# Optimization experiments

Hardware: AMD Instinct MI355X
Metric: run time of the kernel (lower is better)

The kernel has to match this reference:

```python
import jax, jax.numpy as jnp
import numpy as np

N, D, H, E_DIM = 2048, 128, 8, 10
DH = D // H
EPS = 1e-5

def _ln(x, g, b):
    mu = jnp.mean(x, axis=-1, keepdims=True)
    var = jnp.mean((x - mu) ** 2, axis=-1, keepdims=True)
    return (x - mu) / jnp.sqrt(var + EPS) * g + b

def setup_inputs() -> dict:
    key = jax.random.key(0)
    ks = jax.random.split(key, 16)
    E = 65536
    inp = {
        "node_feat": jax.random.normal(ks[0], (N, D), jnp.float32),
        "edge_feat": jax.random.normal(ks[1], (E, E_DIM), jnp.float32),
        "src": jax.random.randint(ks[2], (E,), 0, N, jnp.int32).astype(jnp.int64),
        "dst": jax.random.randint(ks[3], (E,), 0, N, jnp.int32).astype(jnp.int64),
        "Wq": jax.random.normal(ks[4], (D, D), jnp.float32) * 0.02,
        "bq": jnp.zeros((D,), jnp.float32),
        "Wk": jax.random.normal(ks[5], (D, D), jnp.float32) * 0.02,
        "bk": jnp.zeros((D,), jnp.float32),
        "Wv": jax.random.normal(ks[6], (D, D), jnp.float32) * 0.02,
        "bv": jnp.zeros((D,), jnp.float32),
        "Wo": jax.random.normal(ks[7], (D, D), jnp.float32) * 0.02,
        "bo": jnp.zeros((D,), jnp.float32),
        "We": jax.random.normal(ks[8], (E_DIM, H), jnp.float32) * 0.02,
        "be": jnp.zeros((H,), jnp.float32),
        "g1": jnp.ones((D,), jnp.float32),
        "b1n": jnp.zeros((D,), jnp.float32),
        "g2": jnp.ones((D,), jnp.float32),
        "b2n": jnp.zeros((D,), jnp.float32),
        "W1": jax.random.normal(ks[9], (D, 4 * D), jnp.float32) * 0.02,
        "bf1": jnp.zeros((4 * D,), jnp.float32),
        "W2": jax.random.normal(ks[10], (4 * D, D), jnp.float32) * 0.02,
        "bf2": jnp.zeros((D,), jnp.float32),
    }
    return inp

def reference(node_feat, edge_feat, src, dst, Wq, bq, Wk, bk, Wv, bv, Wo, bo,
              We, be, g1, b1n, g2, b2n, W1, bf1, W2, bf2):
    n = node_feat.shape[0]
    Q = (node_feat @ Wq + bq).reshape(n, H, DH)
    K = (node_feat @ Wk + bk).reshape(n, H, DH)
    V = (node_feat @ Wv + bv).reshape(n, H, DH)
    scores = jnp.einsum('ihd,jhd->ijh', Q, K) / jnp.sqrt(jnp.float32(DH))
    # scatter edge bias into dense [N,N,H] (set semantics, like torch indexed assign)
    edge_bias = edge_feat @ We + be  # [E,H]
    bias = jnp.zeros((n, n, H), scores.dtype).at[src, dst].set(edge_bias)
    scores = scores + bias
    # symmetric adjacency mask with self-loops
    adj = jnp.zeros((n, n), scores.dtype)
    adj = adj.at[src, dst].set(1.0).at[dst, src].set(1.0)
    idx = jnp.arange(n)
    adj = adj.at[idx, idx].set(1.0)
    scores = jnp.where(adj[:, :, None] == 0, -jnp.inf, scores)
    attn = jax.nn.softmax(scores, axis=1)  # softmax over keys j (dim=1)
    out = jnp.einsum('ijh,jhd->ihd', attn, V).reshape(n, -1)
    out = out @ Wo + bo
    out = _ln(out + node_feat, g1, b1n)
    ffn = jax.nn.relu(out @ W1 + bf1) @ W2 + bf2
    out = _ln(out + ffn, g2, b2n)
    return out
```

## Files before the change

### kernel.cpp

```cpp
#include <hip/hip_runtime.h>
#include <hip/hip_bf16.h>

#define NN   2048
#define DDIM 128
#define HH   8
#define DHH  16
#define NEDGE 65536
#define FFN  512
#define EPSV 1e-5f
#define CAP  256

typedef const float* fp_c;

__device__ __forceinline__ bool idx64(const int* src) {
    return (src[1] | src[3] | src[5] | src[7] | src[9] | src[11]) == 0;
}

__global__ __launch_bounds__(512) void k_pq(float* Qf, float* Kf, float* Vf, fp_c x,
                                            fp_c Wq, fp_c bq, fp_c Wk, fp_c bk, fp_c Wv, fp_c bv,
                                            int* ewin, unsigned* bm, float* eb,
                                            const int* src, const int* dst,
                                            fp_c edge_feat, fp_c We, fp_c be) {
    int b = blockIdx.x;
    int t = threadIdx.x;
    if (b < 256) {
        __shared__ float sx[8][DDIM];
        __shared__ float redq[4][8][DDIM];
        __shared__ float redk[4][8][DDIM];
        __shared__ float redv[4][8][DDIM];
        int r0 = b * 8;
        int c = t & 127;
        int ks = t >> 7;
        sx[t >> 7][t & 127]       = x[r0 * DDIM + t];
        sx[4 + (t >> 7)][t & 127] = x[r0 * DDIM + 512 + t];
        __syncthreads();
        float aq[8], ak[8], av[8];
#pragma unroll
        for (int r = 0; r < 8; r++) { aq[r] = 0; ak[r] = 0; av[r] = 0; }
        int kbeg = ks * 32;
#pragma unroll 8
        for (int k = kbeg; k < kbeg + 32; k++) {
            float wq = Wq[k * DDIM + c];
            float wk = Wk[k * DDIM + c];
            float wv = Wv[k * DDIM + c];
#pragma unroll
            for (int r = 0; r < 8; r++) {
                float xv = sx[r][k];
                aq[r] += xv * wq; ak[r] += xv * wk; av[r] += xv * wv;
            }
        }
#pragma unroll
        for (int r = 0; r < 8; r++) {
            redq[ks][r][c] = aq[r];
            redk[ks][r][c] = ak[r];
            redv[ks][r][c] = av[r];
        }
        __syncthreads();
        int rr = t >> 7, cc = t & 127;
        float vq0 = 0, vk0 = 0, vv0 = 0, vq1 = 0, vk1 = 0, vv1 = 0;
#pragma unroll
        for (int s = 0; s < 4; s++) {
            vq0 += redq[s][rr][cc];     vk0 += redk[s][rr][cc];     vv0 += redv[s][rr][cc];
            vq1 += redq[s][rr + 4][cc]; vk1 += redk[s][rr + 4][cc]; vv1 += redv[s][rr + 4][cc];
        }
        float vbq = bq[cc], vbk = bk[cc], vbv = bv[cc];
        Qf[(r0 + rr) * DDIM + cc]     = (vq0 + vbq) * 0.25f;
        Kf[(r0 + rr) * DDIM + cc]     = vk0 + vbk;
        Vf[(r0 + rr) * DDIM + cc]     = vv0 + vbv;
        Qf[(r0 + rr + 4) * DDIM + cc] = (vq1 + vbq) * 0.25f;
        Kf[(r0 + rr + 4) * DDIM + cc] = vk1 + vbk;
        Vf[(r0 + rr + 4) * DDIM + cc] = vv1 + vbv;
    } else {
        __shared__ float sWe[80];
        __shared__ float sbe[8];
        if (t < 80) sWe[t] = We[t];
        if (t < 8)  sbe[t] = be[t];
        __syncthreads();
        int u = (b - 256) * 512 + t;
        if (u < NN * 64 / 4) ((int4*)bm)[u] = make_int4(0, 0, 0, 0);
        ((int4*)ewin)[u]         = make_int4(0, 0, 0, 0);
        ((int4*)ewin)[u + 65536] = make_int4(0, 0, 0, 0);
        if (u < NEDGE) {
            float ef[10];
#pragma unroll
            for (int k = 0; k < 10; k++) ef[k] = edge_feat[u * 10 + k];
#pragma unroll
            for (int h = 0; h < 8; h++) {
                float a = sbe[h];
#pragma unroll
                for (int k = 0; k < 10; k++) a += ef[k] * sWe[k * 8 + h];
                eb[u * 8 + h] = a;
            }
        }
    }
}

__global__ __launch_bounds__(512) void k_scatter(unsigned* bm, const int* src, const int* dst) {
    int t = blockIdx.x * blockDim.x + threadIdx.x;
    bool is64 = idx64(src);
    if (t < NEDGE) {
        int s = is64 ? src[2 * t] : src[t];
        int d = is64 ? dst[2 * t] : dst[t];
        atomicOr(&bm[s * 64 + (d >> 5)], 1u << (d & 31));
        atomicOr(&bm[d * 64 + (s >> 5)], 1u << (s & 31));
    } else if (t < NEDGE + NN) {
        int i = t - NEDGE;
        atomicOr(&bm[i * 64 + (i >> 5)], 1u << (i & 31));
    }
}

__global__ __launch_bounds__(512) void k_rank(int* ewin, const unsigned* bm,
                                              const int* src, const int* dst) {
    int e = blockIdx.x * blockDim.x + threadIdx.x;
    if (e >= NEDGE) return;
    bool is64 = idx64(src);
    int s = is64 ? src[2 * e] : src[e];
    int d = is64 ? dst[2 * e] : dst[e];
    const unsigned* row = bm + s * 64;
    int dw = d >> 5;
    int rank = __popc(row[dw] & ((1u << (d & 31)) - 1u));
    for (int w = 0; w < dw; w++) rank += __popc(row[w]);
    atomicMax(&ewin[s * CAP + rank], e + 1);
}

__global__ __launch_bounds__(256) void k_attn(float* attn_out, const float* Qf, const float* Kf,
                                              const float* Vf, const int* ewin, const float* eb,
                                              const unsigned* bm) {
    __shared__ float qrow[DDIM];
    __shared__ int   lj[CAP + 8];
    __shared__ int   lev[CAP + 8];
    __shared__ float sc[CAP + 8][HH];
    __shared__ float hinv[HH];
    __shared__ float redpv[2][DDIM];
    __shared__ int   scnt;
    int i = blockIdx.x;
    int t = threadIdx.x;
    if (t < 128) qrow[t] = Qf[i * DDIM + t];

    if (t < 64) {
        unsigned word = bm[i * 64 + t];
        int pc = __popc(word);
        int x = pc;
#pragma unroll
        for (int off = 1; off < 64; off <<= 1) {
            int y = __shfl_up(x, off);
            if (t >= off) x += y;
        }
        int cnt = __shfl(x, 63);
        if (cnt > CAP - 8) cnt = CAP - 8;
        int idx = x - pc;
        unsigned w = word;
        while (w && idx < CAP) {
            int bpos = __ffs(w) - 1;
            lj[idx++] = (t << 5) + bpos;
            w &= w - 1;
        }
        if (t < 8) lj[cnt + t] = 0;
        if (t == 0) scnt = cnt;
    }
    __syncthreads();
    int cnt = scnt;
    int cnt8 = (cnt + 7) & ~7;
    if (t < cnt8) lev[t] = (t < cnt) ? (ewin[i * CAP + t] - 1) : -1;
    __syncthreads();

    int h = t & 7;
    int nsl = t >> 3;
    const float4* q4 = (const float4*)(qrow + h * DHH);
    float4 q0 = q4[0], q1 = q4[1], q2 = q4[2], q3 = q4[3];
    for (int n = nsl; n < cnt8; n += 32) {
        int j = lj[n];
        const float4* k4 = (const float4*)(Kf + j * DDIM + h * DHH);
        float4 k0 = k4[0], k1 = k4[1], k2 = k4[2], k3 = k4[3];
        float s = q0.x * k0.x + q0.y * k0.y + q0.z * k0.z + q0.w * k0.w
                + q1.x * k1.x + q1.y * k1.y + q1.z * k1.z + q1.w * k1.w
                + q2.x * k2.x + q2.y * k2.y + q2.z * k2.z + q2.w * k2.w
                + q3.x * k3.x + q3.y * k3.y + q3.z * k3.z + q3.w * k3.w;
        int ev = lev[n];
        if (ev >= 0) s += eb[ev * 8 + h];
        sc[n][h] = s;
    }
    __syncthreads();

    {
        int hh = t >> 5;
        int sub = t & 31;
        float m = -1e30f;
        for (int n = sub; n < cnt; n += 32) m = fmaxf(m, sc[n][hh]);
#pragma unroll
        for (int off = 1; off < 32; off <<= 1) m = fmaxf(m, __shfl_xor(m, off));
        float ssum = 0.f;
        for (int n = sub; n < cnt; n += 32) {
            float e = __expf(sc[n][hh] - m);
            sc[n][hh] = e;
            ssum += e;
        }
#pragma unroll
        for (int off = 1; off < 32; off <<= 1) ssum += __shfl_xor(ssum, off);
        if (sub == 0) hinv[hh] = 1.0f / ssum;
    }
    if (t < 64) {
        int p = cnt + (t >> 3);
        if (p < cnt8) sc[p][t & 7] = 0.f;
    }
    __syncthreads();

    {
        int g = t >> 7, c = t & 127, h2 = c >> 4;
        float a = 0.f;
#pragma unroll 4
        for (int n = g; n < cnt8; n += 2)
            a += sc[n][h2] * Vf[lj[n] * DDIM + c];
        redpv[g][c] = a;
    }
    __syncthreads();
    if (t < 128)
        attn_out[i * DDIM + t] = (redpv[0][t] + redpv[1][t]) * hinv[t >> 4];
}

__global__ __launch_bounds__(512) void k_tail(float* out, const float* ain,
                                              fp_c Wo, fp_c bo, fp_c node, fp_c g1, fp_c b1,
                                              fp_c W1, fp_c bf1, fp_c W2, fp_c bf2,
                                              fp_c g2, fp_c b2) {
    __shared__ float sa[8][DDIM];
    __shared__ float red[4][8][DDIM];
    __shared__ float x1ld[8][DDIM];
    __shared__ float sh[8][FFN];
    __shared__ float4 sc4[8];
    int t = threadIdx.x;
    int r0 = blockIdx.x * 8;
    int c = t & 127;
    int ks = t >> 7;
    int rr = t >> 7, cc = t & 127;
    sa[t >> 7][t & 127]       = ain[r0 * DDIM + t];
    sa[4 + (t >> 7)][t & 127] = ain[r0 * DDIM + 512 + t];
    __syncthreads();

    {
        float acc[8] = {0, 0, 0, 0, 0, 0, 0, 0};
        int kbeg = ks * 32;
#pragma unroll 8
        for (int k = kbeg; k < kbeg + 32; k++) {
            float w = Wo[k * DDIM + c];
#pragma unroll
            for (int r = 0; r < 8; r++) acc[r] += sa[r][k] * w;
        }
#pragma unroll
        for (int r = 0; r < 8; r++) red[ks][r][c] = acc[r];
        __syncthreads();
        float bov = bo[cc];
        float val0 = red[0][rr][cc] + red[1][rr][cc] + red[2][rr][cc] + red[3][rr][cc]
                   + bov + node[(r0 + rr) * DDIM + cc];
        float val1 = red[0][rr + 4][cc] + red[1][rr + 4][cc] + red[2][rr + 4][cc] + red[3][rr + 4][cc]
                   + bov + node[(r0 + rr + 4) * DDIM + cc];
        float4 v = make_float4(val0, val0 * val0, val1, val1 * val1);
#pragma unroll
        for (int off = 32; off >= 1; off >>= 1) {
            v.x += __shfl_down(v.x, off);
            v.y += __shfl_down(v.y, off);
            v.z += __shfl_down(v.z, off);
            v.w += __shfl_down(v.w, off);
        }
        if ((t & 63) == 0) sc4[t >> 6] = v;
        __syncthreads();
        float gv = g1[cc], bv = b1[cc];
        {
            float sum = sc4[2 * rr].x + sc4[2 * rr + 1].x;
            float sq  = sc4[2 * rr].y + sc4[2 * rr + 1].y;
            float mu = sum * (1.0f / DDIM);
            float var = sq * (1.0f / DDIM) - mu * mu;
            x1ld[rr][cc] = (val0 - mu) * rsqrtf(var + EPSV) * gv + bv;
        }
        {
            float sum = sc4[2 * rr].z + sc4[2 * rr + 1].z;
            float sq  = sc4[2 * rr].w + sc4[2 * rr + 1].w;
            float mu = sum * (1.0f / DDIM);
            float var = sq * (1.0f / DDIM) - mu * mu;
            x1ld[rr + 4][cc] = (val1 - mu) * rsqrtf(var + EPSV) * gv + bv;
        }
    }
    __syncthreads();

    {
        float acc[8] = {0, 0, 0, 0, 0, 0, 0, 0};
#pragma unroll 4
        for (int k = 0; k < DDIM; k++) {
            float w = W1[k * FFN + t];
#pragma unroll
            for (int r = 0; r < 8; r++) acc[r] += x1ld[r][k] * w;
        }
        float bb = bf1[t];
#pragma unroll
        for (int r = 0; r < 8; r++) sh[r][t] = fmaxf(acc[r] + bb, 0.f);
    }
    __syncthreads();

    {
        float acc[8] = {0, 0, 0, 0, 0, 0, 0, 0};
        int kbeg = ks * 128;
#pragma unroll 8
        for (int k = kbeg; k < kbeg + 128; k++) {
            float w = W2[k * DDIM + c];
#pragma unroll
            for (int r = 0; r < 8; r++) acc[r] += sh[r][k] * w;
        }
#pragma unroll
        for (int r = 0; r < 8; r++) red[ks][r][c] = acc[r];
        __syncthreads();
        float bv2 = bf2[cc];
        float val0 = red[0][rr][cc] + red[1][rr][cc] + red[2][rr][cc] + red[3][rr][cc]
                   + bv2 + x1ld[rr][cc];
        float val1 = red[0][rr + 4][cc] + red[1][rr + 4][cc] + red[2][rr + 4][cc] + red[3][rr + 4][cc]
                   + bv2 + x1ld[rr + 4][cc];
        float4 v = make_float4(val0, val0 * val0, val1, val1 * val1);
#pragma unroll
        for (int off = 32; off >= 1; off >>= 1) {
            v.x += __shfl_down(v.x, off);
            v.y += __shfl_down(v.y, off);
            v.z += __shfl_down(v.z, off);
            v.w += __shfl_down(v.w, off);
        }
        if ((t & 63) == 0) sc4[t >> 6] = v;
        __syncthreads();
        float gv = g2[cc], bv = b2[cc];
        {
            float sum = sc4[2 * rr].x + sc4[2 * rr + 1].x;
            float sq  = sc4[2 * rr].y + sc4[2 * rr + 1].y;
            float mu = sum * (1.0f / DDIM);
            float var = sq * (1.0f / DDIM) - mu * mu;
            out[(r0 + rr) * DDIM + cc] = (val0 - mu) * rsqrtf(var + EPSV) * gv + bv;
        }
        {
            float sum = sc4[2 * rr].z + sc4[2 * rr + 1].z;
            float sq  = sc4[2 * rr].w + sc4[2 * rr + 1].w;
            float mu = sum * (1.0f / DDIM);
            float var = sq * (1.0f / DDIM) - mu * mu;
            out[(r0 + rr + 4) * DDIM + cc] = (val1 - mu) * rsqrtf(var + EPSV) * gv + bv;
        }
    }
}

extern "C" void kernel_launch(void* const* d_in, const int* in_sizes, int n_in,
                              void* d_out, int out_size, void* d_ws, size_t ws_size,
                              hipStream_t stream) {
    fp_c node = (fp_c)d_in[0];
    fp_c edge_feat = (fp_c)d_in[1];
    const int* src = (const int*)d_in[2];
    const int* dst = (const int*)d_in[3];
    fp_c Wq = (fp_c)d_in[4];  fp_c bq = (fp_c)d_in[5];
    fp_c Wk = (fp_c)d_in[6];  fp_c bk = (fp_c)d_in[7];
    fp_c Wv = (fp_c)d_in[8];  fp_c bv = (fp_c)d_in[9];
    fp_c Wo = (fp_c)d_in[10]; fp_c bo = (fp_c)d_in[11];
    fp_c We = (fp_c)d_in[12]; fp_c be = (fp_c)d_in[13];
    fp_c g1 = (fp_c)d_in[14]; fp_c b1n = (fp_c)d_in[15];
    fp_c g2 = (fp_c)d_in[16]; fp_c b2n = (fp_c)d_in[17];
    fp_c W1 = (fp_c)d_in[18]; fp_c bf1 = (fp_c)d_in[19];
    fp_c W2 = (fp_c)d_in[20]; fp_c bf2 = (fp_c)d_in[21];

    char* ws = (char*)d_ws;
    int* ewin     = (int*)ws;      ws += (size_t)NN * CAP * 4;
    unsigned* bm  = (unsigned*)ws; ws += (size_t)NN * 64 * 4;
    float* eb     = (float*)ws;    ws += (size_t)NEDGE * 8 * 4;
    float* Qf     = (float*)ws;    ws += (size_t)NN * DDIM * 4;
    float* Kf     = (float*)ws;    ws += (size_t)NN * DDIM * 4;
    float* Vf     = (float*)ws;    ws += (size_t)NN * DDIM * 4;
    float* attn_o = (float*)ws;    ws += (size_t)NN * DDIM * 4;

    k_pq<<<384, 512, 0, stream>>>(Qf, Kf, Vf, node, Wq, bq, Wk, bk, Wv, bv,
                                  ewin, bm, eb, src, dst, edge_feat, We, be);
    k_scatter<<<(NEDGE + NN + 511) / 512, 512, 0, stream>>>(bm, src, dst);
    k_rank<<<NEDGE / 512, 512, 0, stream>>>(ewin, bm, src, dst);
    k_attn<<<NN, 256, 0, stream>>>(attn_o, Qf, Kf, Vf, ewin, eb, bm);
    k_tail<<<NN / 8, 512, 0, stream>>>((float*)d_out, attn_o, Wo, bo, node, g1, b1n,
                                       W1, bf1, W2, bf2, g2, b2n);
}
```

Before: 81.33 us.

## Fuse all stages into one cooperative persistent kernel with dense edge-id table

```diff
diff --git a/kernel.cpp b/kernel.cpp
--- a/kernel.cpp
+++ b/kernel.cpp
@@ -1,258 +1,231 @@
 #include <hip/hip_runtime.h>
 #include <hip/hip_bf16.h>
-
-#define NN   2048
-#define DDIM 128
-#define HH   8
-#define DHH  16
+#include <hip/hip_cooperative_groups.h>
+
+namespace cg = cooperative_groups;
+
+#define NN    2048
+#define DDIM  128
+#define HH    8
+#define DHH   16
 #define NEDGE 65536
-#define FFN  512
-#define EPSV 1e-5f
-#define CAP  256
-
-typedef const float* fp_c;
+#define FFN   512
+#define EPSV  1e-5f
+#define CAP   256
+#define NBLK  256
+#define NTHR  512
+
+struct Params {
+    const float *node, *edge_feat;
+    const int *src, *dst;
+    const float *Wq, *bq, *Wk, *bk, *Wv, *bv, *Wo, *bo, *We, *be;
+    const float *g1, *b1n, *g2n, *b2n, *W1, *bf1, *W2, *bf2;
+    float *Qf, *Kf, *Vf, *out;
+    int* eid;
+    unsigned* bm;
+    float* eb;
+};
+
+union Smem {
+    struct { float sx[8][DDIM]; float rq[4][8][DDIM]; float rk[4][8][DDIM];
+             float rv[4][8][DDIM]; } q;
+    struct { float qrow[2][DDIM]; int lj[2][CAP + 8]; int lev[2][CAP + 8];
+             float sc[2][CAP + 8][HH]; float hinv[2][HH];
+             float redpv[2][2][DDIM]; int scnt[2]; } a;
+    struct { float red[4][8][DDIM]; float x1[8][DDIM]; float sh[8][FFN];
+             float4 sc4[8]; } tl;
+};
+struct Pers { float ao[8][DDIM]; };
 
 __device__ __forceinline__ bool idx64(const int* src) {
     return (src[1] | src[3] | src[5] | src[7] | src[9] | src[11]) == 0;
 }
 
-__global__ __launch_bounds__(512) void k_pq(float* Qf, float* Kf, float* Vf, fp_c x,
-                                            fp_c Wq, fp_c bq, fp_c Wk, fp_c bk, fp_c Wv, fp_c bv,
-                                            int* ewin, unsigned* bm, float* eb,
-                                            const int* src, const int* dst,
-                                            fp_c edge_feat, fp_c We, fp_c be) {
-    int b = blockIdx.x;
-    int t = threadIdx.x;
-    if (b < 256) {
-        __shared__ float sx[8][DDIM];
-        __shared__ float redq[4][8][DDIM];
-        __shared__ float redk[4][8][DDIM];
-        __shared__ float redv[4][8][DDIM];
-        int r0 = b * 8;
-        int c = t & 127;
-        int ks = t >> 7;
-        sx[t >> 7][t & 127]       = x[r0 * DDIM + t];
-        sx[4 + (t >> 7)][t & 127] = x[r0 * DDIM + 512 + t];
-        __syncthreads();
-        float aq[8], ak[8], av[8];
-#pragma unroll
-        for (int r = 0; r < 8; r++) { aq[r] = 0; ak[r] = 0; av[r] = 0; }
-        int kbeg = ks * 32;
+__device__ __forceinline__ void phase_pq(const Params& P, int b, int t, Smem& S, bool is64) {
+    int g = b * NTHR + t;
+    if (g < NN * 64 / 4) ((int4*)P.bm)[g] = make_int4(0, 0, 0, 0);
+    if (g < NN) P.eid[(long)g * NN + g] = -2;
+    if (g < NEDGE) {
+        int s = is64 ? P.src[2 * g] : P.src[g];
+        int d = is64 ? P.dst[2 * g] : P.dst[g];
+        P.eid[(long)s * NN + d] = -2;
+        P.eid[(long)d * NN + s] = -2;
+        float ef[10];
+#pragma unroll
+        for (int k = 0; k < 10; k++) ef[k] = P.edge_feat[g * 10 + k];
+#pragma unroll
+        for (int h = 0; h < 8; h++) {
+            float a = P.be[h];
+#pragma unroll
+            for (int k = 0; k < 10; k++) a += ef[k] * P.We[k * 8 + h];
+            P.eb[g * 8 + h] = a;
+        }
+    }
+    int r0 = b * 8, c = t & 127, ks = t >> 7;
+    S.q.sx[ks][c]     = P.node[r0 * DDIM + t];
+    S.q.sx[4 + ks][c] = P.node[r0 * DDIM + 512 + t];
+    __syncthreads();
+    float aq[8], ak[8], av[8];
+#pragma unroll
+    for (int r = 0; r < 8; r++) { aq[r] = 0; ak[r] = 0; av[r] = 0; }
+    int kbeg = ks * 32;
 #pragma unroll 8
-        for (int k = kbeg; k < kbeg + 32; k++) {
-            float wq = Wq[k * DDIM + c];
-            float wk = Wk[k * DDIM + c];
-            float wv = Wv[k * DDIM + c];
-#pragma unroll
-            for (int r = 0; r < 8; r++) {
-                float xv = sx[r][k];
-                aq[r] += xv * wq; ak[r] += xv * wk; av[r] += xv * wv;
+    for (int k = kbeg; k < kbeg + 32; k++) {
+        float wq = P.Wq[k * DDIM + c];
+        float wk = P.Wk[k * DDIM + c];
+        float wv = P.Wv[k * DDIM + c];
+#pragma unroll
+        for (int r = 0; r < 8; r++) {
+            float xv = S.q.sx[r][k];
+            aq[r] += xv * wq; ak[r] += xv * wk; av[r] += xv * wv;
+        }
+    }
+#pragma unroll
+    for (int r = 0; r < 8; r++) {
+        S.q.rq[ks][r][c] = aq[r];
+        S.q.rk[ks][r][c] = ak[r];
+        S.q.rv[ks][r][c] = av[r];
+    }
+    __syncthreads();
+    int rr = t >> 7, cc = t & 127;
+    float vq0 = 0, vk0 = 0, vv0 = 0, vq1 = 0, vk1 = 0, vv1 = 0;
+#pragma unroll
+    for (int s = 0; s < 4; s++) {
+        vq0 += S.q.rq[s][rr][cc];     vk0 += S.q.rk[s][rr][cc];     vv0 += S.q.rv[s][rr][cc];
+        vq1 += S.q.rq[s][rr + 4][cc]; vk1 += S.q.rk[s][rr + 4][cc]; vv1 += S.q.rv[s][rr + 4][cc];
+    }
+    float vbq = P.bq[cc], vbk = P.bk[cc], vbv = P.bv[cc];
+    P.Qf[(r0 + rr) * DDIM + cc]     = (vq0 + vbq) * 0.25f;
+    P.Kf[(r0 + rr) * DDIM + cc]     = vk0 + vbk;
+    P.Vf[(r0 + rr) * DDIM + cc]     = vv0 + vbv;
+    P.Qf[(r0 + rr + 4) * DDIM + cc] = (vq1 + vbq) * 0.25f;
+    P.Kf[(r0 + rr + 4) * DDIM + cc] = vk1 + vbk;
+    P.Vf[(r0 + rr + 4) * DDIM + cc] = vv1 + vbv;
+}
+
+__device__ __forceinline__ void phase_scatter(const Params& P, int b, int t, bool is64) {
+    int g = b * NTHR + t;
+    if (g < NEDGE) {
+        int s = is64 ? P.src[2 * g] : P.src[g];
+        int d = is64 ? P.dst[2 * g] : P.dst[g];
+        atomicOr(&P.bm[s * 64 + (d >> 5)], 1u << (d & 31));
+        atomicOr(&P.bm[d * 64 + (s >> 5)], 1u << (s & 31));
+        atomicMax(&P.eid[(long)s * NN + d], g);
+    } else if (g < NEDGE + NN) {
+        int i = g - NEDGE;
+        atomicOr(&P.bm[i * 64 + (i >> 5)], 1u << (i & 31));
+    }
+}
+
+__device__ __forceinline__ void phase_attn(const Params& P, int b, int t, Smem& S, Pers& Pr) {
+    int gi = t >> 8;
+    int t2 = t & 255;
+#pragma unroll 1
+    for (int p = 0; p < 4; p++) {
+        __syncthreads();
+        int il = p * 2 + gi;
+        int i = b * 8 + il;
+        if (t2 < 128) S.a.qrow[gi][t2] = P.Qf[i * DDIM + t2];
+        if (t2 < 64) {
+            unsigned word = P.bm[i * 64 + t2];
+            int pc = __popc(word);
+            int x = pc;
+#pragma unroll
+            for (int off = 1; off < 64; off <<= 1) {
+                int y = __shfl_up(x, off);
+                if (t2 >= off) x += y;
             }
-        }
-#pragma unroll
-        for (int r = 0; r < 8; r++) {
-            redq[ks][r][c] = aq[r];
-            redk[ks][r][c] = ak[r];
-            redv[ks][r][c] = av[r];
-        }
-        __syncthreads();
-        int rr = t >> 7, cc = t & 127;
-        float vq0 = 0, vk0 = 0, vv0 = 0, vq1 = 0, vk1 = 0, vv1 = 0;
-#pragma unroll
-        for (int s = 0; s < 4; s++) {
-            vq0 += redq[s][rr][cc];     vk0 += redk[s][rr][cc];     vv0 += redv[s][rr][cc];
-            vq1 += redq[s][rr + 4][cc]; vk1 += redk[s][rr + 4][cc]; vv1 += redv[s][rr + 4][cc];
-        }
-        float vbq = bq[cc], vbk = bk[cc], vbv = bv[cc];
-        Qf[(r0 + rr) * DDIM + cc]     = (vq0 + vbq) * 0.25f;
-        Kf[(r0 + rr) * DDIM + cc]     = vk0 + vbk;
-        Vf[(r0 + rr) * DDIM + cc]     = vv0 + vbv;
-        Qf[(r0 + rr + 4) * DDIM + cc] = (vq1 + vbq) * 0.25f;
-        Kf[(r0 + rr + 4) * DDIM + cc] = vk1 + vbk;
-        Vf[(r0 + rr + 4) * DDIM + cc] = vv1 + vbv;
-    } else {
-        __shared__ float sWe[80];
-        __shared__ float sbe[8];
-        if (t < 80) sWe[t] = We[t];
-        if (t < 8)  sbe[t] = be[t];
-        __syncthreads();
-        int u = (b - 256) * 512 + t;
-        if (u < NN * 64 / 4) ((int4*)bm)[u] = make_int4(0, 0, 0, 0);
-        ((int4*)ewin)[u]         = make_int4(0, 0, 0, 0);
-        ((int4*)ewin)[u + 65536] = make_int4(0, 0, 0, 0);
-        if (u < NEDGE) {
-            float ef[10];
-#pragma unroll
-            for (int k = 0; k < 10; k++) ef[k] = edge_feat[u * 10 + k];
-#pragma unroll
-            for (int h = 0; h < 8; h++) {
-                float a = sbe[h];
-#pragma unroll
-                for (int k = 0; k < 10; k++) a += ef[k] * sWe[k * 8 + h];
-                eb[u * 8 + h] = a;
+            int cnt = __shfl(x, 63);
+            if (cnt > CAP - 8) cnt = CAP - 8;
+            int idx = x - pc;
+            unsigned w = word;
+            while (w && idx < CAP) {
+                int bp = __ffs(w) - 1;
+                S.a.lj[gi][idx++] = (t2 << 5) + bp;
+                w &= w - 1;
             }
-        }
-    }
-}
-
-__global__ __launch_bounds__(512) void k_scatter(unsigned* bm, const int* src, const int* dst) {
-    int t = blockIdx.x * blockDim.x + threadIdx.x;
-    bool is64 = idx64(src);
-    if (t < NEDGE) {
-        int s = is64 ? src[2 * t] : src[t];
-        int d = is64 ? dst[2 * t] : dst[t];
-        atomicOr(&bm[s * 64 + (d >> 5)], 1u << (d & 31));
-        atomicOr(&bm[d * 64 + (s >> 5)], 1u << (s & 31));
-    } else if (t < NEDGE + NN) {
-        int i = t - NEDGE;
-        atomicOr(&bm[i * 64 + (i >> 5)], 1u << (i & 31));
-    }
-}
-
-__global__ __launch_bounds__(512) void k_rank(int* ewin, const unsigned* bm,
-                                              const int* src, const int* dst) {
-    int e = blockIdx.x * blockDim.x + threadIdx.x;
-    if (e >= NEDGE) return;
-    bool is64 = idx64(src);
-    int s = is64 ? src[2 * e] : src[e];
-    int d = is64 ? dst[2 * e] : dst[e];
-    const unsigned* row = bm + s * 64;
-    int dw = d >> 5;
-    int rank = __popc(row[dw] & ((1u << (d & 31)) - 1u));
-    for (int w = 0; w < dw; w++) rank += __popc(row[w]);
-    atomicMax(&ewin[s * CAP + rank], e + 1);
-}
-
-__global__ __launch_bounds__(256) void k_attn(float* attn_out, const float* Qf, const float* Kf,
-                                              const float* Vf, const int* ewin, const float* eb,
-                                              const unsigned* bm) {
-    __shared__ float qrow[DDIM];
-    __shared__ int   lj[CAP + 8];
-    __shared__ int   lev[CAP + 8];
-    __shared__ float sc[CAP + 8][HH];
-    __shared__ float hinv[HH];
-    __shared__ float redpv[2][DDIM];
-    __shared__ int   scnt;
-    int i = blockIdx.x;
-    int t = threadIdx.x;
-    if (t < 128) qrow[t] = Qf[i * DDIM + t];
-
-    if (t < 64) {
-        unsigned word = bm[i * 64 + t];
-        int pc = __popc(word);
-        int x = pc;
-#pragma unroll
-        for (int off = 1; off < 64; off <<= 1) {
-            int y = __shfl_up(x, off);
-            if (t >= off) x += y;
-        }
-        int cnt = __shfl(x, 63);
-        if (cnt > CAP - 8) cnt = CAP - 8;
-        int idx = x - pc;
-        unsigned w = word;
-        while (w && idx < CAP) {
-            int bpos = __ffs(w) - 1;
-            lj[idx++] = (t << 5) + bpos;
-            w &= w - 1;
-        }
-        if (t < 8) lj[cnt + t] = 0;
-        if (t == 0) scnt = cnt;
-    }
-    __syncthreads();
-    int cnt = scnt;
-    int cnt8 = (cnt + 7) & ~7;
-    if (t < cnt8) lev[t] = (t < cnt) ? (ewin[i * CAP + t] - 1) : -1;
-    __syncthreads();
-
-    int h = t & 7;
-    int nsl = t >> 3;
-    const float4* q4 = (const float4*)(qrow + h * DHH);
-    float4 q0 = q4[0], q1 = q4[1], q2 = q4[2], q3 = q4[3];
-    for (int n = nsl; n < cnt8; n += 32) {
-        int j = lj[n];
-        const float4* k4 = (const float4*)(Kf + j * DDIM + h * DHH);
-        float4 k0 = k4[0], k1 = k4[1], k2 = k4[2], k3 = k4[3];
-        float s = q0.x * k0.x + q0.y * k0.y + q0.z * k0.z + q0.w * k0.w
-                + q1.x * k1.x + q1.y * k1.y + q1.z * k1.z + q1.w * k1.w
-                + q2.x * k2.x + q2.y * k2.y + q2.z * k2.z + q2.w * k2.w
-                + q3.x * k3.x + q3.y * k3.y + q3.z * k3.z + q3.w * k3.w;
-        int ev = lev[n];
-        if (ev >= 0) s += eb[ev * 8 + h];
-        sc[n][h] = s;
-    }
-    __syncthreads();
-
-    {
-        int hh = t >> 5;
-        int sub = t & 31;
-        float m = -1e30f;
-        for (int n = sub; n < cnt; n += 32) m = fmaxf(m, sc[n][hh]);
-#pragma unroll
-        for (int off = 1; off < 32; off <<= 1) m = fmaxf(m, __shfl_xor(m, off));
-        float ssum = 0.f;
-        for (int n = sub; n < cnt; n += 32) {
-            float e = __expf(sc[n][hh] - m);
-            sc[n][hh] = e;
-            ssum += e;
-        }
-#pragma unroll
-        for (int off = 1; off < 32; off <<= 1) ssum += __shfl_xor(ssum, off);
-        if (sub == 0) hinv[hh] = 1.0f / ssum;
-    }
-    if (t < 64) {
-        int p = cnt + (t >> 3);
-        if (p < cnt8) sc[p][t & 7] = 0.f;
-    }
-    __syncthreads();
-
-    {
-        int g = t >> 7, c = t & 127, h2 = c >> 4;
-        float a = 0.f;
+            if (t2 < 8) S.a.lj[gi][cnt + t2] = 0;
+            if (t2 == 0) S.a.scnt[gi] = cnt;
+        }
+        __syncthreads();
+        int cnt = S.a.scnt[gi];
+        int cnt8 = (cnt + 7) & ~7;
+        if (t2 < cnt8)
+            S.a.lev[gi][t2] = (t2 < cnt) ? P.eid[(long)i * NN + S.a.lj[gi][t2]] : -1;
+        __syncthreads();
+        {
+            int h = t2 & 7, nsl = t2 >> 3;
+            const float4* q4 = (const float4*)(&S.a.qrow[gi][h * DHH]);
+            float4 q0 = q4[0], q1 = q4[1], q2 = q4[2], q3 = q4[3];
+            for (int n = nsl; n < cnt8; n += 32) {
+                int j = S.a.lj[gi][n];
+                const float4* k4 = (const float4*)(P.Kf + j * DDIM + h * DHH);
+                float4 k0 = k4[0], k1 = k4[1], k2 = k4[2], k3 = k4[3];
+                float s = q0.x * k0.x + q0.y * k0.y + q0.z * k0.z + q0.w * k0.w
+                        + q1.x * k1.x + q1.y * k1.y + q1.z * k1.z + q1.w * k1.w
+                        + q2.x * k2.x + q2.y * k2.y + q2.z * k2.z + q2.w * k2.w
+                        + q3.x * k3.x + q3.y * k3.y + q3.z * k3.z + q3.w * k3.w;
+                int ev = S.a.lev[gi][n];
+                if (ev >= 0) s += P.eb[ev * 8 + h];
+                S.a.sc[gi][n][h] = s;
+            }
+        }
+        __syncthreads();
+        {
+            int hh = t2 >> 5, sub = t2 & 31;
+            float m = -1e30f;
+            for (int n = sub; n < cnt; n += 32) m = fmaxf(m, S.a.sc[gi][n][hh]);
+#pragma unroll
+            for (int off = 1; off < 32; off <<= 1) m = fmaxf(m, __shfl_xor(m, off));
+            float ssum = 0.f;
+            for (int n = sub; n < cnt; n += 32) {
+                float e = __expf(S.a.sc[gi][n][hh] - m);
+                S.a.sc[gi][n][hh] = e;
+                ssum += e;
+            }
+#pragma unroll
+            for (int off = 1; off < 32; off <<= 1) ssum += __shfl_xor(ssum, off);
+            if (sub == 0) S.a.hinv[gi][hh] = 1.0f / ssum;
+        }
+        if (t2 < 64) {
+            int pp = cnt + (t2 >> 3);
+            if (pp < cnt8) S.a.sc[gi][pp][t2 & 7] = 0.f;
+        }
+        __syncthreads();
+        {
+            int gg = t2 >> 7, c = t2 & 127, h2 = c >> 4;
+            float a = 0.f;
 #pragma unroll 4
-        for (int n = g; n < cnt8; n += 2)
-            a += sc[n][h2] * Vf[lj[n] * DDIM + c];
-        redpv[g][c] = a;
-    }
-    __syncthreads();
-    if (t < 128)
-        attn_out[i * DDIM + t] = (redpv[0][t] + redpv[1][t]) * hinv[t >> 4];
-}
-
-__global__ __launch_bounds__(512) void k_tail(float* out, const float* ain,
-                                              fp_c Wo, fp_c bo, fp_c node, fp_c g1, fp_c b1,
-                                              fp_c W1, fp_c bf1, fp_c W2, fp_c bf2,
-                                              fp_c g2, fp_c b2) {
-    __shared__ float sa[8][DDIM];
-    __shared__ float red[4][8][DDIM];
-    __shared__ float x1ld[8][DDIM];
-    __shared__ float sh[8][FFN];
-    __shared__ float4 sc4[8];
-    int t = threadIdx.x;
-    int r0 = blockIdx.x * 8;
-    int c = t & 127;
-    int ks = t >> 7;
+            for (int n = gg; n < cnt8; n += 2)
+                a += S.a.sc[gi][n][h2] * P.Vf[S.a.lj[gi][n] * DDIM + c];
+            S.a.redpv[gi][gg][c] = a;
+        }
+        __syncthreads();
+        if (t2 < 128)
+            Pr.ao[il][t2] = (S.a.redpv[gi][0][t2] + S.a.redpv[gi][1][t2]) * S.a.hinv[gi][t2 >> 4];
+    }
+}
+
+__device__ __forceinline__ void phase_tail(const Params& P, int b, int t, Smem& S, Pers& Pr) {
+    int r0 = b * 8, c = t & 127, ks = t >> 7;
     int rr = t >> 7, cc = t & 127;
-    sa[t >> 7][t & 127]       = ain[r0 * DDIM + t];
-    sa[4 + (t >> 7)][t & 127] = ain[r0 * DDIM + 512 + t];
-    __syncthreads();
-
     {
         float acc[8] = {0, 0, 0, 0, 0, 0, 0, 0};
         int kbeg = ks * 32;
 #pragma unroll 8
         for (int k = kbeg; k < kbeg + 32; k++) {
-            float w = Wo[k * DDIM + c];
-#pragma unroll
-            for (int r = 0; r < 8; r++) acc[r] += sa[r][k] * w;
-        }
-#pragma unroll
-        for (int r = 0; r < 8; r++) red[ks][r][c] = acc[r];
-        __syncthreads();
-        float bov = bo[cc];
-        float val0 = red[0][rr][cc] + red[1][rr][cc] + red[2][rr][cc] + red[3][rr][cc]
-                   + bov + node[(r0 + rr) * DDIM + cc];
-        float val1 = red[0][rr + 4][cc] + red[1][rr + 4][cc] + red[2][rr + 4][cc] + red[3][rr + 4][cc]
-                   + bov + node[(r0 + rr + 4) * DDIM + cc];
+            float w = P.Wo[k * DDIM + c];
+#pragma unroll
+            for (int r = 0; r < 8; r++) acc[r] += Pr.ao[r][k] * w;
+        }
+#pragma unroll
+        for (int r = 0; r < 8; r++) S.tl.red[ks][r][c] = acc[r];
+        __syncthreads();
+        float bov = P.bo[cc];
+        float val0 = S.tl.red[0][rr][cc] + S.tl.red[1][rr][cc] + S.tl.red[2][rr][cc]
+                   + S.tl.red[3][rr][cc] + bov + P.node[(r0 + rr) * DDIM + cc];
+        float val1 = S.tl.red[0][rr + 4][cc] + S.tl.red[1][rr + 4][cc] + S.tl.red[2][rr + 4][cc]
+                   + S.tl.red[3][rr + 4][cc] + bov + P.node[(r0 + rr + 4) * DDIM + cc];
         float4 v = make_float4(val0, val0 * val0, val1, val1 * val1);
 #pragma unroll
         for (int off = 32; off >= 1; off >>= 1) {
@@ -261,57 +234,56 @@
             v.z += __shfl_down(v.z, off);
             v.w += __shfl_down(v.w, off);
         }
-        if ((t & 63) == 0) sc4[t >> 6] = v;
-        __syncthreads();
-        float gv = g1[cc], bv = b1[cc];
-        {
-            float sum = sc4[2 * rr].x + sc4[2 * rr + 1].x;
-            float sq  = sc4[2 * rr].y + sc4[2 * rr + 1].y;
+        if ((t & 63) == 0) S.tl.sc4[t >> 6] = v;
+        __syncthreads();
+        float gv = P.g1[cc], bv = P.b1n[cc];
+        {
+            float sum = S.tl.sc4[2 * rr].x + S.tl.sc4[2 * rr + 1].x;
+            float sq  = S.tl.sc4[2 * rr].y + S.tl.sc4[2 * rr + 1].y;
             float mu = sum * (1.0f / DDIM);
             float var = sq * (1.0f / DDIM) - mu * mu;
-            x1ld[rr][cc] = (val0 - mu) * rsqrtf(var + EPSV) * gv + bv;
-        }
-        {
-            float sum = sc4[2 * rr].z + sc4[2 * rr + 1].z;
-            float sq  = sc4[2 * rr].w + sc4[2 * rr + 1].w;
+            S.tl.x1[rr][cc] = (val0 - mu) * rsqrtf(var + EPSV) * gv + bv;
+        }
+        {
+            float sum = S.tl.sc4[2 * rr].z + S.tl.sc4[2 * rr + 1].z;
+            float sq  = S.tl.sc4[2 * rr].w + S.tl.sc4[2 * rr + 1].w;
             float mu = sum * (1.0f / DDIM);
             float var = sq * (1.0f / DDIM) - mu * mu;
-            x1ld[rr + 4][cc] = (val1 - mu) * rsqrtf(var + EPSV) * gv + bv;
-        }
-    }
-    __syncthreads();
-
+            S.tl.x1[rr + 4][cc] = (val1 - mu) * rsqrtf(var + EPSV) * gv + bv;
+        }
+    }
+    __syncthreads();
     {
         float acc[8] = {0, 0, 0, 0, 0, 0, 0, 0};
 #pragma unroll 4
         for (int k = 0; k < DDIM; k++) {
-            float w = W1[k * FFN + t];
-#pragma unroll
-            for (int r = 0; r < 8; r++) acc[r] += x1ld[r][k] * w;
-        }
-        float bb = bf1[t];
-#pragma unroll
-        for (int r = 0; r < 8; r++) sh[r][t] = fmaxf(acc[r] + bb, 0.f);
-    }
-    __syncthreads();
-
+            float w = P.W1[k * FFN + t];
+#pragma unroll
+            for (int r = 0; r < 8; r++) acc[r] += S.tl.x1[r][k] * w;
+        }
+        float bb = P.bf1[t];
+#pragma unroll
+        for (int r = 0; r < 8; r++) S.tl.sh[r][t] = fmaxf(acc[r] + bb, 0.f);
+    }
+    __syncthreads();
     {
         float acc[8] = {0, 0, 0, 0, 0, 0, 0, 0};
         int kbeg = ks * 128;
 #pragma unroll 8
         for (int k = kbeg; k < kbeg + 128; k++) {
-            float w = W2[k * DDIM + c];
-#pragma unroll
-            for (int r = 0; r < 8; r++) acc[r] += sh[r][k] * w;
-        }
-#pragma unroll
-        for (int r = 0; r < 8; r++) red[ks][r][c] = acc[r];
-        __syncthreads();
-        float bv2 = bf2[cc];
-        float val0 = red[0][rr][cc] + red[1][rr][cc] + red[2][rr][cc] + red[3][rr][cc]
-                   + bv2 + x1ld[rr][cc];
-        float val1 = red[0][rr + 4][cc] + red[1][rr + 4][cc] + red[2][rr + 4][cc] + red[3][rr + 4][cc]
-                   + bv2 + x1ld[rr + 4][cc];
+            float w = P.W2[k * DDIM + c];
+#pragma unroll
+            for (int r = 0; r < 8; r++) acc[r] += S.tl.sh[r][k] * w;
+        }
+        __syncthreads();
+#pragma unroll
+        for (int r = 0; r < 8; r++) S.tl.red[ks][r][c] = acc[r];
+        __syncthreads();
+        float bv2 = P.bf2[cc];
+        float val0 = S.tl.red[0][rr][cc] + S.tl.red[1][rr][cc] + S.tl.red[2][rr][cc]
+                   + S.tl.red[3][rr][cc] + bv2 + S.tl.x1[rr][cc];
+        float val1 = S.tl.red[0][rr + 4][cc] + S.tl.red[1][rr + 4][cc] + S.tl.red[2][rr + 4][cc]
+                   + S.tl.red[3][rr + 4][cc] + bv2 + S.tl.x1[rr + 4][cc];
         float4 v = make_float4(val0, val0 * val0, val1, val1 * val1);
 #pragma unroll
         for (int off = 32; off >= 1; off >>= 1) {
@@ -320,57 +292,97 @@
             v.z += __shfl_down(v.z, off);
             v.w += __shfl_down(v.w, off);
         }
-        if ((t & 63) == 0) sc4[t >> 6] = v;
-        __syncthreads();
-        float gv = g2[cc], bv = b2[cc];
-        {
-            float sum = sc4[2 * rr].x + sc4[2 * rr + 1].x;
-            float sq  = sc4[2 * rr].y + sc4[2 * rr + 1].y;
+        if ((t & 63) == 0) S.tl.sc4[t >> 6] = v;
+        __syncthreads();
+        float gv = P.g2n[cc], bv = P.b2n[cc];
+        {
+            float sum = S.tl.sc4[2 * rr].x + S.tl.sc4[2 * rr + 1].x;
+            float sq  = S.tl.sc4[2 * rr].y + S.tl.sc4[2 * rr + 1].y;
             float mu = sum * (1.0f / DDIM);
             float var = sq * (1.0f / DDIM) - mu * mu;
-            out[(r0 + rr) * DDIM + cc] = (val0 - mu) * rsqrtf(var + EPSV) * gv + bv;
-        }
-        {
-            float sum = sc4[2 * rr].z + sc4[2 * rr + 1].z;
-            float sq  = sc4[2 * rr].w + sc4[2 * rr + 1].w;
+            P.out[(r0 + rr) * DDIM + cc] = (val0 - mu) * rsqrtf(var + EPSV) * gv + bv;
+        }
+        {
+            float sum = S.tl.sc4[2 * rr].z + S.tl.sc4[2 * rr + 1].z;
+            float sq  = S.tl.sc4[2 * rr].w + S.tl.sc4[2 * rr + 1].w;
             float mu = sum * (1.0f / DDIM);
             float var = sq * (1.0f / DDIM) - mu * mu;
-            out[(r0 + rr + 4) * DDIM + cc] = (val1 - mu) * rsqrtf(var + EPSV) * gv + bv;
-        }
-    }
+            P.out[(r0 + rr + 4) * DDIM + cc] = (val1 - mu) * rsqrtf(var + EPSV) * gv + bv;
+        }
+    }
+}
+
+__global__ __launch_bounds__(NTHR, 2) void k_mega(Params P) {
+    __shared__ Smem S;
+    __shared__ Pers Pr;
+    int b = blockIdx.x, t = threadIdx.x;
+    bool is64 = idx64(P.src);
+    phase_pq(P, b, t, S, is64);
+    cg::this_grid().sync();
+    phase_scatter(P, b, t, is64);
+    cg::this_grid().sync();
+    phase_attn(P, b, t, S, Pr);
+    __syncthreads();
+    phase_tail(P, b, t, S, Pr);
+}
+
+__global__ __launch_bounds__(NTHR, 2) void k_f1(Params P) {
+    __shared__ Smem S;
+    phase_pq(P, blockIdx.x, threadIdx.x, S, idx64(P.src));
+}
+__global__ __launch_bounds__(NTHR, 2) void k_f2(Params P) {
+    phase_scatter(P, blockIdx.x, threadIdx.x, idx64(P.src));
+}
+__global__ __launch_bounds__(NTHR, 2) void k_f3(Params P) {
+    __shared__ Smem S;
+    __shared__ Pers Pr;
+    phase_attn(P, blockIdx.x, threadIdx.x, S, Pr);
+    __syncthreads();
+    phase_tail(P, blockIdx.x, threadIdx.x, S, Pr);
 }
 
 extern "C" void kernel_launch(void* const* d_in, const int* in_sizes, int n_in,
                               void* d_out, int out_size, void* d_ws, size_t ws_size,
                               hipStream_t stream) {
-    fp_c node = (fp_c)d_in[0];
-    fp_c edge_feat = (fp_c)d_in[1];
-    const int* src = (const int*)d_in[2];
-    const int* dst = (const int*)d_in[3];
-    fp_c Wq = (fp_c)d_in[4];  fp_c bq = (fp_c)d_in[5];
-    fp_c Wk = (fp_c)d_in[6];  fp_c bk = (fp_c)d_in[7];
-    fp_c Wv = (fp_c)d_in[8];  fp_c bv = (fp_c)d_in[9];
-    fp_c Wo = (fp_c)d_in[10]; fp_c bo = (fp_c)d_in[11];
-    fp_c We = (fp_c)d_in[12]; fp_c be = (fp_c)d_in[13];
-    fp_c g1 = (fp_c)d_in[14]; fp_c b1n = (fp_c)d_in[15];
-    fp_c g2 = (fp_c)d_in[16]; fp_c b2n = (fp_c)d_in[17];
-    fp_c W1 = (fp_c)d_in[18]; fp_c bf1 = (fp_c)d_in[19];
-    fp_c W2 = (fp_c)d_in[20]; fp_c bf2 = (fp_c)d_in[21];
+    Params P;
+    P.node      = (const float*)d_in[0];
+    P.edge_feat = (const float*)d_in[1];
+    P.src = (const int*)d_in[2];
+    P.dst = (const int*)d_in[3];
+    P.Wq = (const float*)d_in[4];   P.bq = (const float*)d_in[5];
+    P.Wk = (const float*)d_in[6];   P.bk = (const float*)d_in[7];
+    P.Wv = (const float*)d_in[8];   P.bv = (const float*)d_in[9];
+    P.Wo = (const float*)d_in[10];  P.bo = (const float*)d_in[11];
+    P.We = (const float*)d_in[12];  P.be = (const float*)d_in[13];
+    P.g1 = (const float*)d_in[14];  P.b1n = (const float*)d_in[15];
+    P.g2n = (const float*)d_in[16]; P.b2n = (const float*)d_in[17];
+    P.W1 = (const float*)d_in[18];  P.bf1 = (const float*)d_in[19];
+    P.W2 = (const float*)d_in[20];  P.bf2 = (const float*)d_in[21];
 
     char* ws = (char*)d_ws;
-    int* ewin     = (int*)ws;      ws += (size_t)NN * CAP * 4;
-    unsigned* bm  = (unsigned*)ws; ws += (size_t)NN * 64 * 4;
-    float* eb     = (float*)ws;    ws += (size_t)NEDGE * 8 * 4;
-    float* Qf     = (float*)ws;    ws += (size_t)NN * DDIM * 4;
-    float* Kf     = (float*)ws;    ws += (size_t)NN * DDIM * 4;
-    float* Vf     = (float*)ws;    ws += (size_t)NN * DDIM * 4;
-    float* attn_o = (float*)ws;    ws += (size_t)NN * DDIM * 4;
-
-    k_pq<<<384, 512, 0, stream>>>(Qf, Kf, Vf, node, Wq, bq, Wk, bk, Wv, bv,
-                                  ewin, bm, eb, src, dst, edge_feat, We, be);
-    k_scatter<<<(NEDGE + NN + 511) / 512, 512, 0, stream>>>(bm, src, dst);
-    k_rank<<<NEDGE / 512, 512, 0, stream>>>(ewin, bm, src, dst);
-    k_attn<<<NN, 256, 0, stream>>>(attn_o, Qf, Kf, Vf, ewin, eb, bm);
-    k_tail<<<NN / 8, 512, 0, stream>>>((float*)d_out, attn_o, Wo, bo, node, g1, b1n,
-                                       W1, bf1, W2, bf2, g2, b2n);
-}
+    P.eid = (int*)ws;      ws += (size_t)NN * NN * 4;
+    P.bm  = (unsigned*)ws; ws += (size_t)NN * 64 * 4;
+    P.eb  = (float*)ws;    ws += (size_t)NEDGE * 8 * 4;
+    P.Qf  = (float*)ws;    ws += (size_t)NN * DDIM * 4;
+    P.Kf  = (float*)ws;    ws += (size_t)NN * DDIM * 4;
+    P.Vf  = (float*)ws;    ws += (size_t)NN * DDIM * 4;
+    P.out = (float*)d_out;
+
+    int dev = 0;
+    hipGetDevice(&dev);
+    int coop = 0;
+    hipDeviceGetAttribute(&coop, hipDeviceAttributeCooperativeLaunch, dev);
+
+    bool done = false;
+    if (coop) {
+        void* args[] = { &P };
+        hipError_t e = hipLaunchCooperativeKernel(reinterpret_cast<void*>(k_mega),
+                                                  dim3(NBLK), dim3(NTHR), args, 0, stream);
+        done = (e == hipSuccess);
+    }
+    if (!done) {
+        k_f1<<<NBLK, NTHR, 0, stream>>>(P);
+        k_f2<<<NBLK, NTHR, 0, stream>>>(P);
+        k_f3<<<NBLK, NTHR, 0, stream>>>(P);
+    }
+}
```

Result: slower. 144.6 us (+77.8%).
